# Kernel tuning notes

Measured on AMD Instinct MI355X. Metric: run time of the kernel, lower is better.

## Reference

```python
import jax, jax.numpy as jnp
import numpy as np
import math

H = 768          # bert hidden size
N_HYPO = 384     # number of hyponym instance embeddings
N_HYPER = 384    # number of hypernym instance embeddings
NUM_LABELS = 3


def setup_inputs() -> dict:
    key = jax.random.key(0)
    k1, k2, k3 = jax.random.split(key, 3)
    return {
        "hypo_embeddings": jax.random.normal(k1, (N_HYPO, H), dtype=jnp.float32),
        "hyper_embeddings": jax.random.normal(k2, (N_HYPER, H), dtype=jnp.float32),
        "W_cls": jax.random.normal(k3, (NUM_LABELS, 4 * H), dtype=jnp.float32) * 0.02,
        "b_cls": jnp.zeros((NUM_LABELS,), dtype=jnp.float32),
    }


def reference(hypo_embeddings, hyper_embeddings, W_cls, b_cls):
    h = hypo_embeddings.shape[-1]
    inv_sqrt_h = 1.0 / math.sqrt(h)
    # elementwise outer-product attention score: tanh(x_i * y_j) summed over hidden
    # [n_hypo, n_hyper, h] intermediate -> [n_hypo, n_hyper]
    att = jnp.tanh(hypo_embeddings[:, None, :] * hyper_embeddings[None, :, :]).sum(-1) * inv_sqrt_h

    hypo_side_att = jax.nn.softmax(att, axis=-1)   # rows attend over hypers
    hyper_side_att = jax.nn.softmax(att, axis=0)   # cols attend over hypos

    hyper_typ = hypo_side_att.sum(axis=0)
    hyper_typ = hyper_typ / hyper_typ.sum()
    hypo_typ = hyper_side_att.sum(axis=-1)
    hypo_typ = hypo_typ / hypo_typ.sum()

    # typicalness-weighted prototype pooling
    hyper_prototype = jnp.einsum('nm,md,n->d', hypo_side_att, hyper_embeddings, hypo_typ)
    hypo_prototype = jnp.einsum('nm,nd,m->d', hyper_side_att, hypo_embeddings, hyper_typ)

    feats = jnp.concatenate([
        hyper_prototype,
        hypo_prototype,
        hyper_prototype - hypo_prototype,
        hyper_prototype * hypo_prototype,
    ])  # [4h]
    sub_pred = W_cls @ feats + b_cls  # [num_labels]
    return sub_pred
```

## Files before the change

### kernel.cpp

```cpp
#include <hip/hip_runtime.h>
#include <hip/hip_bf16.h>

#define NN 384
#define HH 768
#define HP 772
#define L2E 1.4426950408889634f
#define TWO_L2E 2.8853900817779268f
#define INV_SQRT_H 0.03608439182435161f

__device__ __forceinline__ float exp2_hw(float x) { return __builtin_amdgcn_exp2f(x); }
__device__ __forceinline__ float rcp_hw(float x) { return __builtin_amdgcn_rcpf(x); }

__global__ __launch_bounds__(256) void k_att(const float* __restrict__ X,
                                             const float* __restrict__ Y,
                                             float* __restrict__ att,
                                             float* __restrict__ attT,
                                             unsigned* __restrict__ bar) {
    __shared__ float xs[8 * HP];
    __shared__ float ys[8 * HP];
    __shared__ float part[4][64];
    const int tid = threadIdx.x;
    const int i0 = blockIdx.y * 8, j0 = blockIdx.x * 8;

    if (blockIdx.x == 0 && blockIdx.y == 0) bar[tid] = 0u;

    const float4* gx = (const float4*)(X + i0 * HH);
    const float4* gy = (const float4*)(Y + j0 * HH);
#pragma unroll
    for (int p = 0; p < 6; p++) {
        int e = tid + p * 256;
        int r = e / 192, c = e - r * 192;
        float4 vx = gx[e];
        float4 vy = gy[e];
        ((float4*)(xs + r * HP))[c] = vx;
        vy.x *= TWO_L2E; vy.y *= TWO_L2E; vy.z *= TWO_L2E; vy.w *= TWO_L2E;
        ((float4*)(ys + r * HP))[c] = vy;
    }
    __syncthreads();

    const int wv = tid >> 6, ln = tid & 63;
    const int i = ln >> 3, j = ln & 7;
    const float4* xr = (const float4*)(xs + i * HP) + wv * 48;
    const float4* yr = (const float4*)(ys + j * HP) + wv * 48;
    float a0 = 0.f, a1 = 0.f, a2 = 0.f, a3 = 0.f;
#pragma unroll 8
    for (int m = 0; m < 48; m++) {
        float4 a = xr[m];
        float4 b = yr[m];
        a0 += rcp_hw(exp2_hw(a.x * b.x) + 1.f);
        a1 += rcp_hw(exp2_hw(a.y * b.y) + 1.f);
        a2 += rcp_hw(exp2_hw(a.z * b.z) + 1.f);
        a3 += rcp_hw(exp2_hw(a.w * b.w) + 1.f);
    }
    part[wv][ln] = (a0 + a1) + (a2 + a3);
    __syncthreads();
    if (tid < 64) {
        float s = part[0][tid] + part[1][tid] + part[2][tid] + part[3][tid];
        int ii = tid >> 3, jj = tid & 7;
        float v = (768.f - 2.f * s) * INV_SQRT_H;
        att[(i0 + ii) * NN + (j0 + jj)] = v;
        attT[(j0 + jj) * NN + (i0 + ii)] = v;
    }
}

__device__ __forceinline__ void grid_bar(unsigned* bar, int idx, unsigned nb) {
    __syncthreads();
    if (threadIdx.x == 0) {
        unsigned* cnt = bar + idx * 64;
        unsigned* flg = cnt + 32;
        __threadfence();
        unsigned old = __hip_atomic_fetch_add(cnt, 1u, __ATOMIC_ACQ_REL, __HIP_MEMORY_SCOPE_AGENT);
        if (old == nb - 1u) {
            __hip_atomic_store(flg, 1u, __ATOMIC_RELEASE, __HIP_MEMORY_SCOPE_AGENT);
        } else {
            while (__hip_atomic_load(flg, __ATOMIC_ACQUIRE, __HIP_MEMORY_SCOPE_AGENT) == 0u) {
                __builtin_amdgcn_s_sleep(4);
            }
        }
        __threadfence();
    }
    __syncthreads();
}

__global__ __launch_bounds__(256) void k_tail(const float* __restrict__ att,
                                              const float* __restrict__ attT,
                                              const float* __restrict__ X,
                                              const float* __restrict__ Y,
                                              const float* __restrict__ W,
                                              const float* __restrict__ bias,
                                              float* rowM, float* rowRS, float* colM, float* colRS,
                                              float* hyper_typ, float* hypo_typ,
                                              float* w_hyper, float* w_hypo,
                                              float* hp, float* hq,
                                              unsigned* bar, float* out) {
    __shared__ float tmp[4];
    __shared__ float red[4][64];
    const int b = blockIdx.x, t = threadIdx.x;
    const unsigned nb = gridDim.x;
    const int wv = t >> 6, ln = t & 63;
    const int gw = (b << 2) + wv;

    for (int it = gw; it < 2 * NN; it += 256) {
        const float* base = (it < NN) ? (att + it * NN) : (attT + (it - NN) * NN);
        float v0 = base[ln], v1 = base[ln + 64], v2 = base[ln + 128];
        float v3 = base[ln + 192], v4 = base[ln + 256], v5 = base[ln + 320];
        float m = fmaxf(fmaxf(fmaxf(v0, v1), fmaxf(v2, v3)), fmaxf(v4, v5));
#pragma unroll
        for (int o = 32; o; o >>= 1) m = fmaxf(m, __shfl_xor(m, o, 64));
        float s = exp2_hw((v0 - m) * L2E) + exp2_hw((v1 - m) * L2E) + exp2_hw((v2 - m) * L2E)
                + exp2_hw((v3 - m) * L2E) + exp2_hw((v4 - m) * L2E) + exp2_hw((v5 - m) * L2E);
#pragma unroll
        for (int o = 32; o; o >>= 1) s += __shfl_xor(s, o, 64);
        if (ln == 0) {
            float rs = 1.f / s;
            if (it < NN) { rowM[it] = m; rowRS[it] = rs; }
            else         { colM[it - NN] = m; colRS[it - NN] = rs; }
        }
    }
    grid_bar(bar, 0, nb);

    for (int it = gw; it < 2 * NN; it += 256) {
        float s = 0.f;
        if (it < NN) {
            const float* base = attT + it * NN;
#pragma unroll
            for (int k = 0; k < 6; k++) {
                int i = ln + 64 * k;
                s += exp2_hw((base[i] - rowM[i]) * L2E) * rowRS[i];
            }
        } else {
            const float* base = att + (it - NN) * NN;
#pragma unroll
            for (int k = 0; k < 6; k++) {
                int j = ln + 64 * k;
                s += exp2_hw((base[j] - colM[j]) * L2E) * colRS[j];
            }
        }
#pragma unroll
        for (int o = 32; o; o >>= 1) s += __shfl_xor(s, o, 64);
        if (ln == 0) {
            if (it < NN) hyper_typ[it] = s * (1.f / NN);
            else         hypo_typ[it - NN] = s * (1.f / NN);
        }
    }
    grid_bar(bar, 1, nb);

    for (int it = gw; it < 2 * NN; it += 256) {
        float s = 0.f;
        if (it < NN) {
            const float* base = attT + it * NN;
#pragma unroll
            for (int k = 0; k < 6; k++) {
                int i = ln + 64 * k;
                s += exp2_hw((base[i] - rowM[i]) * L2E) * rowRS[i] * hypo_typ[i];
            }
        } else {
            const float* base = att + (it - NN) * NN;
#pragma unroll
            for (int k = 0; k < 6; k++) {
                int j = ln + 64 * k;
                s += exp2_hw((base[j] - colM[j]) * L2E) * colRS[j] * hyper_typ[j];
            }
        }
#pragma unroll
        for (int o = 32; o; o >>= 1) s += __shfl_xor(s, o, 64);
        if (ln == 0) {
            if (it < NN) w_hyper[it] = s;
            else         w_hypo[it - NN] = s;
        }
    }
    grid_bar(bar, 2, nb);

    if (b < 24) {
        bool hyper = b < 12;
        int bb = hyper ? b : b - 12;
        int d = bb * 64 + ln;
        float s = 0.f;
        if (hyper) {
            for (int j = wv * 96; j < wv * 96 + 96; j++) s += w_hyper[j] * Y[j * HH + d];
        } else {
            for (int i = wv * 96; i < wv * 96 + 96; i++) s += w_hypo[i] * X[i * HH + d];
        }
        red[wv][ln] = s;
        __syncthreads();
        if (t < 64) {
            float S = red[0][t] + red[1][t] + red[2][t] + red[3][t];
            if (hyper) hp[bb * 64 + t] = S;
            else       hq[bb * 64 + t] = S;
        }
    }
    grid_bar(bar, 3, nb);

    if (b == 0) {
        float acc0 = 0.f, acc1 = 0.f, acc2 = 0.f;
        for (int d = t; d < 4 * HH; d += 256) {
            int seg = d / HH, r = d - seg * HH;
            float f = (seg == 0) ? hp[r] : (seg == 1) ? hq[r] : (seg == 2) ? (hp[r] - hq[r]) : (hp[r] * hq[r]);
            acc0 += W[d] * f;
            acc1 += W[3072 + d] * f;
            acc2 += W[6144 + d] * f;
        }
#pragma unroll
        for (int o = 32; o; o >>= 1) {
            acc0 += __shfl_xor(acc0, o, 64);
            acc1 += __shfl_xor(acc1, o, 64);
            acc2 += __shfl_xor(acc2, o, 64);
        }
        if ((t & 63) == 0) { red[0][t >> 6] = acc0; red[1][t >> 6] = acc1; red[2][t >> 6] = acc2; }
        __syncthreads();
        if (t < 3) {
            float S = red[t][0] + red[t][1] + red[t][2] + red[t][3] + bias[t];
            out[t] = S;
        }
    }
}

extern "C" void kernel_launch(void* const* d_in, const int* in_sizes, int n_in,
                              void* d_out, int out_size, void* d_ws, size_t ws_size,
                              hipStream_t stream) {
    const float* X = (const float*)d_in[0];
    const float* Y = (const float*)d_in[1];
    const float* W = (const float*)d_in[2];
    const float* B = (const float*)d_in[3];
    float* out = (float*)d_out;

    float* ws = (float*)d_ws;
    float* att       = ws;
    float* attT      = att + NN * NN;
    float* rowM      = attT + NN * NN;
    float* rowRS     = rowM + NN;
    float* colM      = rowRS + NN;
    float* colRS     = colM + NN;
    float* hyper_typ = colRS + NN;
    float* hypo_typ  = hyper_typ + NN;
    float* w_hyper   = hypo_typ + NN;
    float* w_hypo    = w_hyper + NN;
    float* hp        = w_hypo + NN;
    float* hq        = hp + HH;
    unsigned* bar    = (unsigned*)(hq + HH);

    k_att<<<dim3(48, 48), 256, 0, stream>>>(X, Y, att, attT, bar);
    k_tail<<<64, 256, 0, stream>>>(att, attT, X, Y, W, B,
                                   rowM, rowRS, colM, colRS,
                                   hyper_typ, hypo_typ, w_hyper, w_hypo,
                                   hp, hq, bar, out);
}
```

Measured before the change: 119.7 us.

## Relax grid barrier ordering, use agent-scope atomics for cross-block data, double tail grid

Replaces the acquire/release fences in the software grid barrier with relaxed atomics and a shorter sleep. Cross-block intermediates are now read and written through relaxed agent-scope atomic loads and stores, so visibility relies on device-coherent accesses instead of fences. The tail kernel launches 128 blocks instead of 64, with the loop strides following the grid size. The aim is lower barrier latency and more parallelism in the softmax phases. The risk is memory-ordering correctness, since relaxed atomics on the barrier counter give no happens-before guarantee for the data written before it.

```diff
diff --git a/kernel.cpp b/kernel.cpp
--- a/kernel.cpp
+++ b/kernel.cpp
@@ -10,6 +10,13 @@
 
 __device__ __forceinline__ float exp2_hw(float x) { return __builtin_amdgcn_exp2f(x); }
 __device__ __forceinline__ float rcp_hw(float x) { return __builtin_amdgcn_rcpf(x); }
+
+__device__ __forceinline__ float ld_nc(const float* p) {
+    return __hip_atomic_load(p, __ATOMIC_RELAXED, __HIP_MEMORY_SCOPE_AGENT);
+}
+__device__ __forceinline__ void st_nc(float* p, float v) {
+    __hip_atomic_store(p, v, __ATOMIC_RELAXED, __HIP_MEMORY_SCOPE_AGENT);
+}
 
 __global__ __launch_bounds__(256) void k_att(const float* __restrict__ X,
                                              const float* __restrict__ Y,
@@ -68,16 +75,14 @@
     if (threadIdx.x == 0) {
         unsigned* cnt = bar + idx * 64;
         unsigned* flg = cnt + 32;
-        __threadfence();
-        unsigned old = __hip_atomic_fetch_add(cnt, 1u, __ATOMIC_ACQ_REL, __HIP_MEMORY_SCOPE_AGENT);
+        unsigned old = __hip_atomic_fetch_add(cnt, 1u, __ATOMIC_RELAXED, __HIP_MEMORY_SCOPE_AGENT);
         if (old == nb - 1u) {
-            __hip_atomic_store(flg, 1u, __ATOMIC_RELEASE, __HIP_MEMORY_SCOPE_AGENT);
-        } else {
-            while (__hip_atomic_load(flg, __ATOMIC_ACQUIRE, __HIP_MEMORY_SCOPE_AGENT) == 0u) {
-                __builtin_amdgcn_s_sleep(4);
-            }
-        }
-        __threadfence();
+            __hip_atomic_store(flg, 1u, __ATOMIC_RELAXED, __HIP_MEMORY_SCOPE_AGENT);
+        } else {
+            while (__hip_atomic_load(flg, __ATOMIC_RELAXED, __HIP_MEMORY_SCOPE_AGENT) == 0u) {
+                __builtin_amdgcn_s_sleep(1);
+            }
+        }
     }
     __syncthreads();
 }
@@ -93,14 +98,14 @@
                                               float* w_hyper, float* w_hypo,
                                               float* hp, float* hq,
                                               unsigned* bar, float* out) {
-    __shared__ float tmp[4];
     __shared__ float red[4][64];
     const int b = blockIdx.x, t = threadIdx.x;
     const unsigned nb = gridDim.x;
     const int wv = t >> 6, ln = t & 63;
     const int gw = (b << 2) + wv;
-
-    for (int it = gw; it < 2 * NN; it += 256) {
+    const int nw = nb << 2;
+
+    for (int it = gw; it < 2 * NN; it += nw) {
         const float* base = (it < NN) ? (att + it * NN) : (attT + (it - NN) * NN);
         float v0 = base[ln], v1 = base[ln + 64], v2 = base[ln + 128];
         float v3 = base[ln + 192], v4 = base[ln + 256], v5 = base[ln + 320];
@@ -113,60 +118,60 @@
         for (int o = 32; o; o >>= 1) s += __shfl_xor(s, o, 64);
         if (ln == 0) {
             float rs = 1.f / s;
-            if (it < NN) { rowM[it] = m; rowRS[it] = rs; }
-            else         { colM[it - NN] = m; colRS[it - NN] = rs; }
+            if (it < NN) { st_nc(rowM + it, m); st_nc(rowRS + it, rs); }
+            else         { st_nc(colM + it - NN, m); st_nc(colRS + it - NN, rs); }
         }
     }
     grid_bar(bar, 0, nb);
 
-    for (int it = gw; it < 2 * NN; it += 256) {
+    for (int it = gw; it < 2 * NN; it += nw) {
         float s = 0.f;
         if (it < NN) {
             const float* base = attT + it * NN;
 #pragma unroll
             for (int k = 0; k < 6; k++) {
                 int i = ln + 64 * k;
-                s += exp2_hw((base[i] - rowM[i]) * L2E) * rowRS[i];
+                s += exp2_hw((base[i] - ld_nc(rowM + i)) * L2E) * ld_nc(rowRS + i);
             }
         } else {
             const float* base = att + (it - NN) * NN;
 #pragma unroll
             for (int k = 0; k < 6; k++) {
                 int j = ln + 64 * k;
-                s += exp2_hw((base[j] - colM[j]) * L2E) * colRS[j];
+                s += exp2_hw((base[j] - ld_nc(colM + j)) * L2E) * ld_nc(colRS + j);
             }
         }
 #pragma unroll
         for (int o = 32; o; o >>= 1) s += __shfl_xor(s, o, 64);
         if (ln == 0) {
-            if (it < NN) hyper_typ[it] = s * (1.f / NN);
-            else         hypo_typ[it - NN] = s * (1.f / NN);
+            if (it < NN) st_nc(hyper_typ + it, s * (1.f / NN));
+            else         st_nc(hypo_typ + it - NN, s * (1.f / NN));
         }
     }
     grid_bar(bar, 1, nb);
 
-    for (int it = gw; it < 2 * NN; it += 256) {
+    for (int it = gw; it < 2 * NN; it += nw) {
         float s = 0.f;
         if (it < NN) {
             const float* base = attT + it * NN;
 #pragma unroll
             for (int k = 0; k < 6; k++) {
                 int i = ln + 64 * k;
-                s += exp2_hw((base[i] - rowM[i]) * L2E) * rowRS[i] * hypo_typ[i];
+                s += exp2_hw((base[i] - ld_nc(rowM + i)) * L2E) * ld_nc(rowRS + i) * ld_nc(hypo_typ + i);
             }
         } else {
             const float* base = att + (it - NN) * NN;
 #pragma unroll
             for (int k = 0; k < 6; k++) {
                 int j = ln + 64 * k;
-                s += exp2_hw((base[j] - colM[j]) * L2E) * colRS[j] * hyper_typ[j];
+                s += exp2_hw((base[j] - ld_nc(colM + j)) * L2E) * ld_nc(colRS + j) * ld_nc(hyper_typ + j);
             }
         }
 #pragma unroll
         for (int o = 32; o; o >>= 1) s += __shfl_xor(s, o, 64);
         if (ln == 0) {
-            if (it < NN) w_hyper[it] = s;
-            else         w_hypo[it - NN] = s;
+            if (it < NN) st_nc(w_hyper + it, s);
+            else         st_nc(w_hypo + it - NN, s);
         }
     }
     grid_bar(bar, 2, nb);
@@ -177,16 +182,16 @@
         int d = bb * 64 + ln;
         float s = 0.f;
         if (hyper) {
-            for (int j = wv * 96; j < wv * 96 + 96; j++) s += w_hyper[j] * Y[j * HH + d];
-        } else {
-            for (int i = wv * 96; i < wv * 96 + 96; i++) s += w_hypo[i] * X[i * HH + d];
+            for (int j = wv * 96; j < wv * 96 + 96; j++) s += ld_nc(w_hyper + j) * Y[j * HH + d];
+        } else {
+            for (int i = wv * 96; i < wv * 96 + 96; i++) s += ld_nc(w_hypo + i) * X[i * HH + d];
         }
         red[wv][ln] = s;
         __syncthreads();
         if (t < 64) {
             float S = red[0][t] + red[1][t] + red[2][t] + red[3][t];
-            if (hyper) hp[bb * 64 + t] = S;
-            else       hq[bb * 64 + t] = S;
+            if (hyper) st_nc(hp + bb * 64 + t, S);
+            else       st_nc(hq + bb * 64 + t, S);
         }
     }
     grid_bar(bar, 3, nb);
@@ -195,7 +200,8 @@
         float acc0 = 0.f, acc1 = 0.f, acc2 = 0.f;
         for (int d = t; d < 4 * HH; d += 256) {
             int seg = d / HH, r = d - seg * HH;
-            float f = (seg == 0) ? hp[r] : (seg == 1) ? hq[r] : (seg == 2) ? (hp[r] - hq[r]) : (hp[r] * hq[r]);
+            float hpv = ld_nc(hp + r), hqv = ld_nc(hq + r);
+            float f = (seg == 0) ? hpv : (seg == 1) ? hqv : (seg == 2) ? (hpv - hqv) : (hpv * hqv);
             acc0 += W[d] * f;
             acc1 += W[3072 + d] * f;
             acc2 += W[6144 + d] * f;
@@ -240,8 +246,8 @@
     unsigned* bar    = (unsigned*)(hq + HH);
 
     k_att<<<dim3(48, 48), 256, 0, stream>>>(X, Y, att, attT, bar);
-    k_tail<<<64, 256, 0, stream>>>(att, attT, X, Y, W, B,
-                                   rowM, rowRS, colM, colRS,
-                                   hyper_typ, hypo_typ, w_hyper, w_hypo,
-                                   hp, hq, bar, out);
-}
+    k_tail<<<128, 256, 0, stream>>>(att, attT, X, Y, W, B,
+                                    rowM, rowRS, colM, colRS,
+                                    hyper_typ, hypo_typ, w_hyper, w_hypo,
+                                    hp, hq, bar, out);
+}
```

New measurement: 104.4 us. -12.8%, faster.
